# Kernel tuning notes

Hardware: AMD Instinct MI355X
Metric: run time of the kernel (lower is better)

Reference implementation:

```python
import jax, jax.numpy as jnp
import numpy as np

EPS = 1e-9


def setup_inputs() -> dict:
    key = jax.random.key(0)
    k1, k2 = jax.random.split(key)
    B, IN, OUT = 16384, 2048, 2048
    x = jax.random.normal(k1, (B, IN), dtype=jnp.float32)
    w = jax.random.normal(k2, (OUT, IN), dtype=jnp.float32)
    # set_weight_norms_to(initial_weight_norm=0.01): rescale each row's L2 norm to 0.01
    wn = jnp.linalg.norm(w, axis=1, keepdims=True)
    weight = 0.01 * w / (wn + 1e-10)
    logprior = jnp.zeros((OUT,), dtype=jnp.float32)
    lamb = jnp.float32(4.0)  # initial_lambda
    return {"x": x, "weight": weight, "logprior": logprior, "lamb": lamb}


def reference(x, weight, logprior, lamb):
    # L2-normalize inputs per row
    x_n = x / (jnp.linalg.norm(x, axis=1, keepdims=True) + EPS)  # [B, IN]
    # L2-normalize weight rows -> cosine similarities
    W = weight / (jnp.linalg.norm(weight, axis=1, keepdims=True) + EPS)  # [OUT, IN]
    a = x_n @ W.T  # [B, OUT] cosine sims
    # RePU inhibition, triangle=False -> setpoint 0
    u = jax.nn.relu(a)
    un = u / (jnp.max(u) + EPS)  # global max normalization
    # power-law with logprior; safe power (0**lamb == 0) to keep grads clean
    pos = un > 0
    ulamb = jnp.where(pos, jnp.where(pos, un, 1.0) ** lamb, 0.0) * jnp.exp(logprior)
    y = ulamb / (jnp.sum(ulamb, axis=1, keepdims=True) + EPS)
    return y
```

## Files before the change

### kernel.cpp

```cpp
#include <hip/hip_runtime.h>
#include <hip/hip_bf16.h>

typedef unsigned short u16;
typedef __attribute__((ext_vector_type(8))) short bf16x8;
typedef __attribute__((ext_vector_type(4))) float f32x4;

#define EPSN 1e-9f


__device__ __forceinline__ u16 f2bf(float f) {
    union { float f; unsigned int u; } c; c.f = f;
    unsigned int u = c.u;
    unsigned int r = (u + 0x7FFFu + ((u >> 16) & 1u)) >> 16;
    return (u16)r;
}

__device__ __forceinline__ void load16_to_lds(const void* g, void* l) {
    __builtin_amdgcn_global_load_lds(
        (const __attribute__((address_space(1))) void*)g,
        (__attribute__((address_space(3))) void*)l,
        16, 0, 0);
}

#define MAXQ 8
__global__ __launch_bounds__(256) void normalize_cast(
    const float* __restrict__ X, u16* __restrict__ Y, int ncols) {
    const size_t row = blockIdx.x;
    const float4* xr = (const float4*)(X + row * (size_t)ncols);
    const int nq = ncols >> 2;

    float4 v[MAXQ];
    float ss = 0.f;
    #pragma unroll
    for (int k = 0; k < MAXQ; ++k) {
        int i = threadIdx.x + k * 256;
        if (i < nq) {
            v[k] = xr[i];
            ss += v[k].x*v[k].x + v[k].y*v[k].y + v[k].z*v[k].z + v[k].w*v[k].w;
        }
    }
    #pragma unroll
    for (int o = 32; o > 0; o >>= 1) ss += __shfl_down(ss, o);

    __shared__ float red[4];
    __shared__ float scale_sh;
    const int lane = threadIdx.x & 63, wv = threadIdx.x >> 6;
    if (lane == 0) red[wv] = ss;
    __syncthreads();
    if (threadIdx.x == 0) {
        float t = red[0] + red[1] + red[2] + red[3];
        scale_sh = 1.f / (sqrtf(t) + EPSN);
    }
    __syncthreads();
    const float s = scale_sh;

    ushort4* yr = (ushort4*)(Y + row * (size_t)ncols);
    #pragma unroll
    for (int k = 0; k < MAXQ; ++k) {
        int i = threadIdx.x + k * 256;
        if (i < nq) {
            ushort4 o4;
            o4.x = f2bf(v[k].x * s); o4.y = f2bf(v[k].y * s);
            o4.z = f2bf(v[k].z * s); o4.w = f2bf(v[k].w * s);
            yr[i] = o4;
        }
    }
}

__global__ void prep_explp(const float* __restrict__ lp, float* __restrict__ out, int n) {
    int i = blockIdx.x * blockDim.x + threadIdx.x;
    if (i < n) out[i] = expf(lp[i]);
}

#define BK 64

__global__ __launch_bounds__(256, 2) void gemm_softhebb(
    const u16* __restrict__ A, const u16* __restrict__ B,
    const float* __restrict__ explp, const float* __restrict__ lambp,
    float* __restrict__ Ul, float* __restrict__ rowsum,
    int M, int N, int K) {
    __shared__ __align__(16) u16 lA[128 * BK];
    __shared__ __align__(16) u16 lB[128 * BK];

    const int tid  = threadIdx.x;
    const int lane = tid & 63;
    const int wm   = (tid >> 6) & 1;
    const int wn   = tid >> 7;
    const int row0 = blockIdx.y * 128;
    const int col0 = blockIdx.x * 128;

    f32x4 acc[4][4] = {};

    const u16* ap[4];
    const u16* bp[4];
    #pragma unroll
    for (int p = 0; p < 4; ++p) {
        int c = p * 256 + tid;
        int r = c >> 3;
        int o = ((c & 7) ^ (r & 7)) * 8;
        ap[p] = A + (size_t)(row0 + r) * K + o;
        bp[p] = B + (size_t)(col0 + r) * K + o;
    }

    for (int k0 = 0; k0 < K; k0 += BK) {
        #pragma unroll
        for (int p = 0; p < 4; ++p) {
            int c = p * 256 + tid;
            load16_to_lds(ap[p] + k0, &lA[c * 8]);
            load16_to_lds(bp[p] + k0, &lB[c * 8]);
        }
        __syncthreads();

        #pragma unroll
        for (int s = 0; s < 2; ++s) {
            const int pos = (((s << 2) + (lane >> 4)) ^ (lane & 7)) * 8;
            bf16x8 af[4], bfr[4];
            #pragma unroll
            for (int i = 0; i < 4; ++i) {
                int r = wm * 64 + i * 16 + (lane & 15);
                af[i] = *(const bf16x8*)&lA[r * 64 + pos];
            }
            #pragma unroll
            for (int j = 0; j < 4; ++j) {
                int r = wn * 64 + j * 16 + (lane & 15);
                bfr[j] = *(const bf16x8*)&lB[r * 64 + pos];
            }
            #pragma unroll
            for (int i = 0; i < 4; ++i)
                #pragma unroll
                for (int j = 0; j < 4; ++j)
                    acc[i][j] = __builtin_amdgcn_mfma_f32_16x16x32_bf16(
                        af[i], bfr[j], acc[i][j], 0, 0, 0);
        }
        __syncthreads();
    }

    const float lam = *lambp;
    const bool lam4 = (lam == 4.0f);
    float el[4];
    #pragma unroll
    for (int j = 0; j < 4; ++j)
        el[j] = explp[col0 + wn * 64 + j * 16 + (lane & 15)];

    #pragma unroll
    for (int i = 0; i < 4; ++i) {
        #pragma unroll
        for (int p = 0; p < 4; ++p) {
            const int m = row0 + wm * 64 + i * 16 + (lane >> 4) * 4 + p;
            float* outrow = Ul + (size_t)m * N + col0 + wn * 64 + (lane & 15);
            float rs = 0.f;
            #pragma unroll
            for (int j = 0; j < 4; ++j) {
                float a = acc[i][j][p];
                float u = 0.f;
                if (a > 0.f) {
                    float pw;
                    if (lam4) { float a2 = a * a; pw = a2 * a2; }
                    else      { pw = __powf(a, lam); }
                    u = pw * el[j];
                }
                outrow[j * 16] = u;
                rs += u;
            }
            rs += __shfl_xor(rs, 1);
            rs += __shfl_xor(rs, 2);
            rs += __shfl_xor(rs, 4);
            rs += __shfl_xor(rs, 8);
            if ((lane & 15) == 0) atomicAdd(&rowsum[m], rs);
        }
    }
}

__global__ __launch_bounds__(256) void finalize_row(
    float* __restrict__ Ul, const float* __restrict__ rowsum, int nq) {
    const size_t row = blockIdx.x;
    const float inv = 1.f / (rowsum[row] + EPSN);
    float4* p = (float4*)(Ul + row * (size_t)nq * 4);
    for (int i = threadIdx.x; i < nq; i += 256) {
        float4 v = p[i];
        v.x *= inv; v.y *= inv; v.z *= inv; v.w *= inv;
        p[i] = v;
    }
}

static inline size_t align256(size_t x) { return (x + 255) & ~(size_t)255; }

extern "C" void kernel_launch(void* const* d_in, const int* in_sizes, int n_in,
                              void* d_out, int out_size, void* d_ws, size_t ws_size,
                              hipStream_t stream) {
    const float* x        = (const float*)d_in[0];
    const float* w        = (const float*)d_in[1];
    const float* logprior = (const float*)d_in[2];
    const float* lamb     = (const float*)d_in[3];
    const int OUT = in_sizes[2];
    const int IN  = in_sizes[1] / OUT;
    const int B   = in_sizes[0] / IN;
    float* out = (float*)d_out;

    char* ws = (char*)d_ws;
    size_t off = 0;
    u16* xn = (u16*)(ws + off);        off += align256((size_t)B * IN * sizeof(u16));
    u16* wn = (u16*)(ws + off);        off += align256((size_t)OUT * IN * sizeof(u16));
    float* rowsum = (float*)(ws + off); off += align256((size_t)B * sizeof(float));
    float* explp  = (float*)(ws + off); off += align256((size_t)OUT * sizeof(float));

    hipMemsetAsync(rowsum, 0, (size_t)B * sizeof(float), stream);
    normalize_cast<<<B, 256, 0, stream>>>(x, xn, IN);
    normalize_cast<<<OUT, 256, 0, stream>>>(w, wn, IN);
    prep_explp<<<(OUT + 255) / 256, 256, 0, stream>>>(logprior, explp, OUT);

    dim3 grid(OUT / 128, B / 128);
    gemm_softhebb<<<grid, 256, 0, stream>>>(xn, wn, explp, lamb, out, rowsum, B, OUT, IN);

    finalize_row<<<B, 256, 0, stream>>>(out, rowsum, OUT / 4);
}
```

Before: 413.5 us.

## Use 256x256 double-buffered GEMM tiles with 8 waves, XCD remap, merged prep kernels

The GEMM moves from 128x128 tiles with 4 waves and a single LDS buffer to 256x256 tiles with 8 waves and double-buffered LDS. Global-to-LDS loads for the next K-tile are issued in quarters, interleaved with the MFMA work and gated by explicit waitcnt/barrier plus s_setprio. A block-index remap groups tiles by XCD for cache locality. The two normalize launches are merged into one, and the exp(logprior) prep kernel is folded into the GEMM epilogue. The aim is more reuse per LDS load, less load latency exposed, and fewer launches, at the cost of 128 KB of LDS and heavier register pressure, which may limit occupancy.

```diff
diff --git a/kernel.cpp b/kernel.cpp
--- a/kernel.cpp
+++ b/kernel.cpp
@@ -23,10 +23,15 @@
 }
 
 #define MAXQ 8
-__global__ __launch_bounds__(256) void normalize_cast(
-    const float* __restrict__ X, u16* __restrict__ Y, int ncols) {
-    const size_t row = blockIdx.x;
-    const float4* xr = (const float4*)(X + row * (size_t)ncols);
+__global__ __launch_bounds__(256) void normalize_cast2(
+    const float* __restrict__ X, const float* __restrict__ W,
+    u16* __restrict__ XO, u16* __restrict__ WO, int ncols, int nxrows) {
+    const int blk = blockIdx.x;
+    const float* src; u16* dst; size_t row;
+    if (blk < nxrows) { src = X; dst = XO; row = blk; }
+    else              { src = W; dst = WO; row = blk - nxrows; }
+
+    const float4* xr = (const float4*)(src + row * (size_t)ncols);
     const int nq = ncols >> 2;
 
     float4 v[MAXQ];
@@ -54,7 +59,7 @@
     __syncthreads();
     const float s = scale_sh;
 
-    ushort4* yr = (ushort4*)(Y + row * (size_t)ncols);
+    ushort4* yr = (ushort4*)(dst + row * (size_t)ncols);
     #pragma unroll
     for (int k = 0; k < MAXQ; ++k) {
         int i = threadIdx.x + k * 256;
@@ -67,72 +72,109 @@
     }
 }
 
-__global__ void prep_explp(const float* __restrict__ lp, float* __restrict__ out, int n) {
-    int i = blockIdx.x * blockDim.x + threadIdx.x;
-    if (i < n) out[i] = expf(lp[i]);
-}
-
-#define BK 64
-
-__global__ __launch_bounds__(256, 2) void gemm_softhebb(
+__global__ __launch_bounds__(512, 2) void gemm_softhebb(
     const u16* __restrict__ A, const u16* __restrict__ B,
-    const float* __restrict__ explp, const float* __restrict__ lambp,
+    const float* __restrict__ logprior, const float* __restrict__ lambp,
     float* __restrict__ Ul, float* __restrict__ rowsum,
     int M, int N, int K) {
-    __shared__ __align__(16) u16 lA[128 * BK];
-    __shared__ __align__(16) u16 lB[128 * BK];
+    __shared__ __align__(16) u16 lA[32768];
+    __shared__ __align__(16) u16 lB[32768];
 
     const int tid  = threadIdx.x;
     const int lane = tid & 63;
-    const int wm   = (tid >> 6) & 1;
-    const int wn   = tid >> 7;
-    const int row0 = blockIdx.y * 128;
-    const int col0 = blockIdx.x * 128;
-
-    f32x4 acc[4][4] = {};
-
-    const u16* ap[4];
-    const u16* bp[4];
-    #pragma unroll
-    for (int p = 0; p < 4; ++p) {
-        int c = p * 256 + tid;
-        int r = c >> 3;
-        int o = ((c & 7) ^ (r & 7)) * 8;
-        ap[p] = A + (size_t)(row0 + r) * K + o;
-        bp[p] = B + (size_t)(col0 + r) * K + o;
-    }
-
-    for (int k0 = 0; k0 < K; k0 += BK) {
+    const int wid  = tid >> 6;
+    const int wm   = wid >> 2;
+    const int wn   = wid & 3;
+
+    const int nwg = gridDim.x;
+    int wg = blockIdx.x;
+    if ((nwg & 7) == 0) {
+        const int cpx = nwg >> 3;
+        wg = (wg & 7) * cpx + (wg >> 3);
+    }
+    const int ntm  = M >> 8;
+    const int tn   = wg / ntm;
+    const int tm   = wg - tn * ntm;
+    const int row0 = tm << 8;
+    const int col0 = tn << 8;
+
+    const u16* gA[2]; const u16* gB[2]; int lo[2];
+    #pragma unroll
+    for (int p = 0; p < 2; ++p) {
+        int n = p * 512 + tid;
+        int r = n >> 2, slot = n & 3;
+        int c = slot ^ ((r >> 1) & 3);
+        gA[p] = A + (size_t)(row0 + r) * K + c * 8;
+        gB[p] = B + (size_t)(col0 + r) * K + c * 8;
+        lo[p] = n * 8;
+    }
+
+    const int sl = ((lane >> 4) ^ ((lane >> 1) & 3)) * 8;
+    int aoff[8], boff[4];
+    #pragma unroll
+    for (int i = 0; i < 8; ++i)
+        aoff[i] = (wm * 128 + i * 16 + (lane & 15)) * 32 + sl;
+    #pragma unroll
+    for (int j = 0; j < 4; ++j)
+        boff[j] = (wn * 64 + j * 16 + (lane & 15)) * 32 + sl;
+
+    f32x4 acc[8][4] = {};
+    bf16x8 af[8];
+
+    const int nt = K >> 6;
+
+    auto stage_half = [&](int buf, int which, int koff) {
+        const int h  = which >> 1;
+        const int go = koff + h * 32;
+        u16* lb = ((which & 1) ? lB : lA) + buf * 16384 + h * 8192;
+        if (which & 1) {
+            load16_to_lds(gB[0] + go, lb + lo[0]);
+            load16_to_lds(gB[1] + go, lb + lo[1]);
+        } else {
+            load16_to_lds(gA[0] + go, lb + lo[0]);
+            load16_to_lds(gA[1] + go, lb + lo[1]);
+        }
+    };
+
+    stage_half(0, 0, 0); stage_half(0, 1, 0); stage_half(0, 2, 0); stage_half(0, 3, 0);
+    asm volatile("s_waitcnt vmcnt(4)" ::: "memory");
+    __builtin_amdgcn_s_barrier();
+
+    for (int t = 0; t < nt; ++t) {
+        const int cur = t & 1;
+        const int nk  = (t + 1 < nt) ? ((t + 1) << 6) : 0;
+        const u16* pA = lA + cur * 16384;
+        const u16* pB = lB + cur * 16384;
+
         #pragma unroll
-        for (int p = 0; p < 4; ++p) {
-            int c = p * 256 + tid;
-            load16_to_lds(ap[p] + k0, &lA[c * 8]);
-            load16_to_lds(bp[p] + k0, &lB[c * 8]);
-        }
-        __syncthreads();
-
-        #pragma unroll
-        for (int s = 0; s < 2; ++s) {
-            const int pos = (((s << 2) + (lane >> 4)) ^ (lane & 7)) * 8;
-            bf16x8 af[4], bfr[4];
+        for (int h = 0; h < 2; ++h) {
+            const u16* phA = pA + h * 8192;
+            const u16* phB = pB + h * 8192;
             #pragma unroll
-            for (int i = 0; i < 4; ++i) {
-                int r = wm * 64 + i * 16 + (lane & 15);
-                af[i] = *(const bf16x8*)&lA[r * 64 + pos];
+            for (int nh = 0; nh < 2; ++nh) {
+                if (nh == 0) {
+                    #pragma unroll
+                    for (int i = 0; i < 8; ++i)
+                        af[i] = *(const bf16x8*)(phA + aoff[i]);
+                }
+                bf16x8 b0 = *(const bf16x8*)(phB + boff[nh * 2 + 0]);
+                bf16x8 b1 = *(const bf16x8*)(phB + boff[nh * 2 + 1]);
+                stage_half(cur ^ 1, h * 2 + nh, nk);
+                __builtin_amdgcn_s_barrier();
+                asm volatile("s_waitcnt lgkmcnt(0)" ::: "memory");
+                __builtin_amdgcn_s_setprio(1);
+                #pragma unroll
+                for (int i = 0; i < 8; ++i) {
+                    acc[i][nh*2+0] = __builtin_amdgcn_mfma_f32_16x16x32_bf16(
+                        af[i], b0, acc[i][nh*2+0], 0, 0, 0);
+                    acc[i][nh*2+1] = __builtin_amdgcn_mfma_f32_16x16x32_bf16(
+                        af[i], b1, acc[i][nh*2+1], 0, 0, 0);
+                }
+                __builtin_amdgcn_s_setprio(0);
+                if (nh == 1) asm volatile("s_waitcnt vmcnt(4)" ::: "memory");
+                __builtin_amdgcn_s_barrier();
             }
-            #pragma unroll
-            for (int j = 0; j < 4; ++j) {
-                int r = wn * 64 + j * 16 + (lane & 15);
-                bfr[j] = *(const bf16x8*)&lB[r * 64 + pos];
-            }
-            #pragma unroll
-            for (int i = 0; i < 4; ++i)
-                #pragma unroll
-                for (int j = 0; j < 4; ++j)
-                    acc[i][j] = __builtin_amdgcn_mfma_f32_16x16x32_bf16(
-                        af[i], bfr[j], acc[i][j], 0, 0, 0);
-        }
-        __syncthreads();
+        }
     }
 
     const float lam = *lambp;
@@ -140,13 +182,13 @@
     float el[4];
     #pragma unroll
     for (int j = 0; j < 4; ++j)
-        el[j] = explp[col0 + wn * 64 + j * 16 + (lane & 15)];
-
-    #pragma unroll
-    for (int i = 0; i < 4; ++i) {
+        el[j] = __expf(logprior[col0 + wn * 64 + j * 16 + (lane & 15)]);
+
+    #pragma unroll
+    for (int i = 0; i < 8; ++i) {
         #pragma unroll
         for (int p = 0; p < 4; ++p) {
-            const int m = row0 + wm * 64 + i * 16 + (lane >> 4) * 4 + p;
+            const int m = row0 + wm * 128 + i * 16 + (lane >> 4) * 4 + p;
             float* outrow = Ul + (size_t)m * N + col0 + wn * 64 + (lane & 15);
             float rs = 0.f;
             #pragma unroll
@@ -202,15 +244,12 @@
     u16* xn = (u16*)(ws + off);        off += align256((size_t)B * IN * sizeof(u16));
     u16* wn = (u16*)(ws + off);        off += align256((size_t)OUT * IN * sizeof(u16));
     float* rowsum = (float*)(ws + off); off += align256((size_t)B * sizeof(float));
-    float* explp  = (float*)(ws + off); off += align256((size_t)OUT * sizeof(float));
 
     hipMemsetAsync(rowsum, 0, (size_t)B * sizeof(float), stream);
-    normalize_cast<<<B, 256, 0, stream>>>(x, xn, IN);
-    normalize_cast<<<OUT, 256, 0, stream>>>(w, wn, IN);
-    prep_explp<<<(OUT + 255) / 256, 256, 0, stream>>>(logprior, explp, OUT);
-
-    dim3 grid(OUT / 128, B / 128);
-    gemm_softhebb<<<grid, 256, 0, stream>>>(xn, wn, explp, lamb, out, rowsum, B, OUT, IN);
+    normalize_cast2<<<B + OUT, 256, 0, stream>>>(x, w, xn, wn, IN, B);
+
+    const int nblk = (B / 256) * (OUT / 256);
+    gemm_softhebb<<<nblk, 512, 0, stream>>>(xn, wn, logprior, lamb, out, rowsum, B, OUT, IN);
 
     finalize_row<<<B, 256, 0, stream>>>(out, rowsum, OUT / 4);
 }
```

Result: no change. 415.0 us (+0.4%).

## Fuse row normalization into persistent GEMM via per-row-tile spin barrier

Applied to the files above, without the earlier changes.

Turns the GEMM into a persistent kernel of 512 blocks that walk the tiles with an XCD-aware remap. After accumulating each tile's row sums atomically, a block waits on a per-row-tile counter until all column tiles of that row band are done, then writes the normalized output directly from registers. This removes the finalize pass, which re-read and re-wrote the whole fp32 output. It also merges the X and W normalize launches into one wave-per-row kernel and computes exp(logprior) inline. The cost is spin-wait stalls, and it relies on all 512 blocks being co-resident (two per CU), otherwise it can deadlock.

```diff
diff --git a/kernel.cpp b/kernel.cpp
--- a/kernel.cpp
+++ b/kernel.cpp
@@ -22,164 +22,174 @@
         16, 0, 0);
 }
 
-#define MAXQ 8
-__global__ __launch_bounds__(256) void normalize_cast(
-    const float* __restrict__ X, u16* __restrict__ Y, int ncols) {
-    const size_t row = blockIdx.x;
-    const float4* xr = (const float4*)(X + row * (size_t)ncols);
+__global__ __launch_bounds__(256) void normalize_cast2(
+    const float* __restrict__ X, const float* __restrict__ W,
+    u16* __restrict__ XO, u16* __restrict__ WO, int ncols, int nxrows, int nrt) {
+    const int lane = threadIdx.x & 63;
+    const int r = blockIdx.x * 4 + (threadIdx.x >> 6);
+    if (r >= nrt) return;
+    const float* src; u16* dst; size_t row;
+    if (r < nxrows) { src = X; dst = XO; row = r; }
+    else            { src = W; dst = WO; row = r - nxrows; }
+
+    const float4* xr = (const float4*)(src + row * (size_t)ncols);
     const int nq = ncols >> 2;
 
-    float4 v[MAXQ];
+    float4 v[8];
     float ss = 0.f;
     #pragma unroll
-    for (int k = 0; k < MAXQ; ++k) {
-        int i = threadIdx.x + k * 256;
+    for (int q = 0; q < 8; ++q) {
+        int i = lane + q * 64;
         if (i < nq) {
-            v[k] = xr[i];
-            ss += v[k].x*v[k].x + v[k].y*v[k].y + v[k].z*v[k].z + v[k].w*v[k].w;
-        }
-    }
-    #pragma unroll
-    for (int o = 32; o > 0; o >>= 1) ss += __shfl_down(ss, o);
-
-    __shared__ float red[4];
-    __shared__ float scale_sh;
-    const int lane = threadIdx.x & 63, wv = threadIdx.x >> 6;
-    if (lane == 0) red[wv] = ss;
-    __syncthreads();
-    if (threadIdx.x == 0) {
-        float t = red[0] + red[1] + red[2] + red[3];
-        scale_sh = 1.f / (sqrtf(t) + EPSN);
-    }
-    __syncthreads();
-    const float s = scale_sh;
-
-    ushort4* yr = (ushort4*)(Y + row * (size_t)ncols);
-    #pragma unroll
-    for (int k = 0; k < MAXQ; ++k) {
-        int i = threadIdx.x + k * 256;
+            v[q] = xr[i];
+            ss += v[q].x*v[q].x + v[q].y*v[q].y + v[q].z*v[q].z + v[q].w*v[q].w;
+        }
+    }
+    #pragma unroll
+    for (int o = 32; o > 0; o >>= 1) ss += __shfl_xor(ss, o);
+    const float s = 1.f / (sqrtf(ss) + EPSN);
+
+    ushort4* yr = (ushort4*)(dst + row * (size_t)ncols);
+    #pragma unroll
+    for (int q = 0; q < 8; ++q) {
+        int i = lane + q * 64;
         if (i < nq) {
             ushort4 o4;
-            o4.x = f2bf(v[k].x * s); o4.y = f2bf(v[k].y * s);
-            o4.z = f2bf(v[k].z * s); o4.w = f2bf(v[k].w * s);
+            o4.x = f2bf(v[q].x * s); o4.y = f2bf(v[q].y * s);
+            o4.z = f2bf(v[q].z * s); o4.w = f2bf(v[q].w * s);
             yr[i] = o4;
         }
     }
 }
-
-__global__ void prep_explp(const float* __restrict__ lp, float* __restrict__ out, int n) {
-    int i = blockIdx.x * blockDim.x + threadIdx.x;
-    if (i < n) out[i] = expf(lp[i]);
-}
-
-#define BK 64
 
 __global__ __launch_bounds__(256, 2) void gemm_softhebb(
     const u16* __restrict__ A, const u16* __restrict__ B,
-    const float* __restrict__ explp, const float* __restrict__ lambp,
-    float* __restrict__ Ul, float* __restrict__ rowsum,
-    int M, int N, int K) {
-    __shared__ __align__(16) u16 lA[128 * BK];
-    __shared__ __align__(16) u16 lB[128 * BK];
+    const float* __restrict__ logprior, const float* __restrict__ lambp,
+    float* __restrict__ Y, float* __restrict__ rowsum, unsigned int* __restrict__ cnt,
+    int M, int N, int K, int iters) {
+    __shared__ __align__(16) u16 lA[128 * 64];
+    __shared__ __align__(16) u16 lB[128 * 64];
 
     const int tid  = threadIdx.x;
     const int lane = tid & 63;
     const int wm   = (tid >> 6) & 1;
     const int wn   = tid >> 7;
-    const int row0 = blockIdx.y * 128;
-    const int col0 = blockIdx.x * 128;
-
-    f32x4 acc[4][4] = {};
-
-    const u16* ap[4];
-    const u16* bp[4];
+    const int ntn  = N >> 7;
+
+    const int nblk = gridDim.x;
+    int b = blockIdx.x;
+    if ((nblk & 7) == 0) b = (b & 7) * (nblk >> 3) + (b >> 3);
+
+    int roff[4], coff[4], lo4[4];
     #pragma unroll
     for (int p = 0; p < 4; ++p) {
         int c = p * 256 + tid;
         int r = c >> 3;
-        int o = ((c & 7) ^ (r & 7)) * 8;
-        ap[p] = A + (size_t)(row0 + r) * K + o;
-        bp[p] = B + (size_t)(col0 + r) * K + o;
-    }
-
-    for (int k0 = 0; k0 < K; k0 += BK) {
-        #pragma unroll
-        for (int p = 0; p < 4; ++p) {
-            int c = p * 256 + tid;
-            load16_to_lds(ap[p] + k0, &lA[c * 8]);
-            load16_to_lds(bp[p] + k0, &lB[c * 8]);
-        }
-        __syncthreads();
-
-        #pragma unroll
-        for (int s = 0; s < 2; ++s) {
-            const int pos = (((s << 2) + (lane >> 4)) ^ (lane & 7)) * 8;
-            bf16x8 af[4], bfr[4];
-            #pragma unroll
-            for (int i = 0; i < 4; ++i) {
-                int r = wm * 64 + i * 16 + (lane & 15);
-                af[i] = *(const bf16x8*)&lA[r * 64 + pos];
-            }
-            #pragma unroll
-            for (int j = 0; j < 4; ++j) {
-                int r = wn * 64 + j * 16 + (lane & 15);
-                bfr[j] = *(const bf16x8*)&lB[r * 64 + pos];
-            }
-            #pragma unroll
-            for (int i = 0; i < 4; ++i)
-                #pragma unroll
-                for (int j = 0; j < 4; ++j)
-                    acc[i][j] = __builtin_amdgcn_mfma_f32_16x16x32_bf16(
-                        af[i], bfr[j], acc[i][j], 0, 0, 0);
-        }
-        __syncthreads();
+        roff[p] = r;
+        coff[p] = ((c & 7) ^ (r & 7)) * 8;
+        lo4[p]  = c * 8;
     }
 
     const float lam = *lambp;
     const bool lam4 = (lam == 4.0f);
-    float el[4];
-    #pragma unroll
-    for (int j = 0; j < 4; ++j)
-        el[j] = explp[col0 + wn * 64 + j * 16 + (lane & 15)];
-
-    #pragma unroll
-    for (int i = 0; i < 4; ++i) {
+
+    for (int it = 0; it < iters; ++it) {
+        const int g   = it * nblk + b;
+        const int tm  = g / ntn;
+        const int tn  = g - tm * ntn;
+        const int row0 = tm << 7;
+        const int col0 = tn << 7;
+
+        f32x4 acc[4][4] = {};
+
+        for (int k0 = 0; k0 < K; k0 += 64) {
+            #pragma unroll
+            for (int p = 0; p < 4; ++p) {
+                load16_to_lds(A + (size_t)(row0 + roff[p]) * K + coff[p] + k0, &lA[lo4[p]]);
+                load16_to_lds(B + (size_t)(col0 + roff[p]) * K + coff[p] + k0, &lB[lo4[p]]);
+            }
+            __syncthreads();
+
+            #pragma unroll
+            for (int s = 0; s < 2; ++s) {
+                const int pos = (((s << 2) + (lane >> 4)) ^ (lane & 7)) * 8;
+                bf16x8 af[4], bfr[4];
+                #pragma unroll
+                for (int i = 0; i < 4; ++i) {
+                    int r = wm * 64 + i * 16 + (lane & 15);
+                    af[i] = *(const bf16x8*)&lA[r * 64 + pos];
+                }
+                #pragma unroll
+                for (int j = 0; j < 4; ++j) {
+                    int r = wn * 64 + j * 16 + (lane & 15);
+                    bfr[j] = *(const bf16x8*)&lB[r * 64 + pos];
+                }
+                #pragma unroll
+                for (int i = 0; i < 4; ++i)
+                    #pragma unroll
+                    for (int j = 0; j < 4; ++j)
+                        acc[i][j] = __builtin_amdgcn_mfma_f32_16x16x32_bf16(
+                            af[i], bfr[j], acc[i][j], 0, 0, 0);
+            }
+            __syncthreads();
+        }
+
+        float el[4];
         #pragma unroll
-        for (int p = 0; p < 4; ++p) {
-            const int m = row0 + wm * 64 + i * 16 + (lane >> 4) * 4 + p;
-            float* outrow = Ul + (size_t)m * N + col0 + wn * 64 + (lane & 15);
-            float rs = 0.f;
-            #pragma unroll
-            for (int j = 0; j < 4; ++j) {
-                float a = acc[i][j][p];
-                float u = 0.f;
-                if (a > 0.f) {
-                    float pw;
-                    if (lam4) { float a2 = a * a; pw = a2 * a2; }
-                    else      { pw = __powf(a, lam); }
-                    u = pw * el[j];
+        for (int j = 0; j < 4; ++j)
+            el[j] = __expf(logprior[col0 + wn * 64 + j * 16 + (lane & 15)]);
+
+        #pragma unroll
+        for (int i = 0; i < 4; ++i) {
+            #pragma unroll
+            for (int p = 0; p < 4; ++p) {
+                const int m = row0 + wm * 64 + i * 16 + (lane >> 4) * 4 + p;
+                float rs = 0.f;
+                #pragma unroll
+                for (int j = 0; j < 4; ++j) {
+                    float a = acc[i][j][p];
+                    float u = 0.f;
+                    if (a > 0.f) {
+                        float pw;
+                        if (lam4) { float a2 = a * a; pw = a2 * a2; }
+                        else      { pw = __powf(a, lam); }
+                        u = pw * el[j];
+                    }
+                    acc[i][j][p] = u;
+                    rs += u;
                 }
-                outrow[j * 16] = u;
-                rs += u;
-            }
-            rs += __shfl_xor(rs, 1);
-            rs += __shfl_xor(rs, 2);
-            rs += __shfl_xor(rs, 4);
-            rs += __shfl_xor(rs, 8);
-            if ((lane & 15) == 0) atomicAdd(&rowsum[m], rs);
-        }
-    }
-}
-
-__global__ __launch_bounds__(256) void finalize_row(
-    float* __restrict__ Ul, const float* __restrict__ rowsum, int nq) {
-    const size_t row = blockIdx.x;
-    const float inv = 1.f / (rowsum[row] + EPSN);
-    float4* p = (float4*)(Ul + row * (size_t)nq * 4);
-    for (int i = threadIdx.x; i < nq; i += 256) {
-        float4 v = p[i];
-        v.x *= inv; v.y *= inv; v.z *= inv; v.w *= inv;
-        p[i] = v;
+                rs += __shfl_xor(rs, 1);
+                rs += __shfl_xor(rs, 2);
+                rs += __shfl_xor(rs, 4);
+                rs += __shfl_xor(rs, 8);
+                if ((lane & 15) == 0) atomicAdd(&rowsum[m], rs);
+            }
+        }
+
+        __threadfence();
+        __syncthreads();
+        if (tid == 0) {
+            atomicAdd(&cnt[tm], 1u);
+            while (__hip_atomic_load(&cnt[tm], __ATOMIC_RELAXED,
+                                     __HIP_MEMORY_SCOPE_AGENT) < (unsigned)ntn)
+                __builtin_amdgcn_s_sleep(2);
+        }
+        __syncthreads();
+        __threadfence();
+
+        #pragma unroll
+        for (int i = 0; i < 4; ++i) {
+            #pragma unroll
+            for (int p = 0; p < 4; ++p) {
+                const int m = row0 + wm * 64 + i * 16 + (lane >> 4) * 4 + p;
+                const float inv = 1.f / (__hip_atomic_load(&rowsum[m], __ATOMIC_RELAXED,
+                                          __HIP_MEMORY_SCOPE_AGENT) + EPSN);
+                float* outrow = Y + (size_t)m * N + col0 + wn * 64 + (lane & 15);
+                #pragma unroll
+                for (int j = 0; j < 4; ++j)
+                    outrow[j * 16] = acc[i][j][p] * inv;
+            }
+        }
     }
 }
 
@@ -197,20 +207,23 @@
     const int B   = in_sizes[0] / IN;
     float* out = (float*)d_out;
 
+    const int ntm = B / 128, ntn = OUT / 128;
+    const int tiles = ntm * ntn;
+
     char* ws = (char*)d_ws;
     size_t off = 0;
-    u16* xn = (u16*)(ws + off);        off += align256((size_t)B * IN * sizeof(u16));
-    u16* wn = (u16*)(ws + off);        off += align256((size_t)OUT * IN * sizeof(u16));
-    float* rowsum = (float*)(ws + off); off += align256((size_t)B * sizeof(float));
-    float* explp  = (float*)(ws + off); off += align256((size_t)OUT * sizeof(float));
-
-    hipMemsetAsync(rowsum, 0, (size_t)B * sizeof(float), stream);
-    normalize_cast<<<B, 256, 0, stream>>>(x, xn, IN);
-    normalize_cast<<<OUT, 256, 0, stream>>>(w, wn, IN);
-    prep_explp<<<(OUT + 255) / 256, 256, 0, stream>>>(logprior, explp, OUT);
-
-    dim3 grid(OUT / 128, B / 128);
-    gemm_softhebb<<<grid, 256, 0, stream>>>(xn, wn, explp, lamb, out, rowsum, B, OUT, IN);
-
-    finalize_row<<<B, 256, 0, stream>>>(out, rowsum, OUT / 4);
-}
+    u16* xn = (u16*)(ws + off);            off += align256((size_t)B * IN * sizeof(u16));
+    u16* wn = (u16*)(ws + off);            off += align256((size_t)OUT * IN * sizeof(u16));
+    float* rowsum = (float*)(ws + off);    off += align256((size_t)B * sizeof(float));
+    unsigned int* cnt = (unsigned int*)(ws + off); off += align256((size_t)ntm * sizeof(unsigned int));
+
+    hipMemsetAsync(rowsum, 0, (size_t)((char*)(cnt + ntm) - (char*)rowsum), stream);
+
+    const int nrt = B + OUT;
+    normalize_cast2<<<(nrt + 3) / 4, 256, 0, stream>>>(x, w, xn, wn, IN, B, nrt);
+
+    const int nblk = 512;
+    const int iters = tiles / nblk;
+    gemm_softhebb<<<nblk, 256, 0, stream>>>(xn, wn, logprior, lamb, out, rowsum, cnt,
+                                            B, OUT, IN, iters);
+}
```

Measured after the change: 724.1 us. 1.75x slower.
